# Kernel tuning notes

Hardware: AMD Instinct MI355X
Metric: run time of the kernel (lower is better)

Reference implementation:

```python
import jax, jax.numpy as jnp
import numpy as np

B = 16384
IN_DIM = 28 * 28
HID = 768
NUM_EXPERTS = 8
NUM_CLASSES = 10
H_PHASOR = 32          # phasor bank harmonics -> 2*H features
DELTA0 = 7.0
DECAY = 0.7            # spiking attention leak
THETA = 1.0
K_WINNERS = 5
TOP_K_ROUTE = 2
TRAITS = (0.6, 0.6, 0.5, 0.5, 0.4)


def setup_inputs() -> dict:
    key = jax.random.key(0)
    ks = jax.random.split(key, 16)
    s = 0.02
    return {
        "x": jax.random.normal(ks[0], (B, 28, 28), jnp.float32),
        "W_in": jax.random.normal(ks[1], (IN_DIM, HID), jnp.float32) * s,
        "b_in": jnp.zeros((HID,), jnp.float32),
        "W_ph": jax.random.normal(ks[2], (2 * H_PHASOR, HID), jnp.float32) * s,
        "b_ph": jnp.zeros((HID,), jnp.float32),
        "W_gate": jax.random.normal(ks[3], (HID, NUM_EXPERTS), jnp.float32) * s,
        "b_gate": jnp.zeros((NUM_EXPERTS,), jnp.float32),
        "W_exp": jax.random.normal(ks[4], (NUM_EXPERTS, HID, HID), jnp.float32) * s,
        "b_exp": jnp.zeros((NUM_EXPERTS, HID), jnp.float32),
        "W_th": jax.random.normal(ks[5], (HID, NUM_EXPERTS), jnp.float32) * s,
        "b_th": jnp.zeros((NUM_EXPERTS,), jnp.float32),
        "W_pm": jax.random.normal(ks[6], (5, NUM_EXPERTS), jnp.float32) * s,
        "b_pm": jnp.zeros((NUM_EXPERTS,), jnp.float32),
        "W_out": jax.random.normal(ks[7], (HID, NUM_CLASSES), jnp.float32) * s,
        "b_out": jnp.zeros((NUM_CLASSES,), jnp.float32),
    }


def reference(x, W_in, b_in, W_ph, b_ph, W_gate, b_gate, W_exp, b_exp,
              W_th, b_th, W_pm, b_pm, W_out, b_out):
    Bn = x.shape[0]
    x_flat = x.reshape((Bn, -1))
    proj = x_flat @ W_in + b_in                                  # [B, HID]

    # Phasor bank on per-sample mean activation: sin/cos at H harmonics
    x_mean = jnp.mean(proj, axis=-1)                             # [B]
    freqs = DELTA0 * jnp.arange(1, H_PHASOR + 1, dtype=proj.dtype)
    phase = x_mean[:, None] * freqs[None, :]                     # [B, H]
    feats = jnp.concatenate([jnp.sin(phase), jnp.cos(phase)], -1)  # [B, 2H]
    enhanced = proj + feats @ W_ph + b_ph                        # [B, HID]

    # Top-K index selection feeding gather/scatter spiking attention
    V = enhanced.shape[-1]
    K = min(32, V)
    topk_idx = jax.lax.top_k(enhanced, K)[1].astype(jnp.int32)   # [B, K]
    w = DECAY ** jnp.arange(K, dtype=enhanced.dtype)             # decaying drive

    def gains_fn(idx):
        v = jnp.zeros((V,), enhanced.dtype).at[idx].add(w)       # scatter-add
        vals, widx = jax.lax.top_k(v, K_WINNERS)                 # k-WTA
        return jnp.ones((V,), enhanced.dtype).at[widx].add(vals / THETA)

    gains = jax.vmap(gains_fn)(topk_idx)                         # [B, V]
    attended = enhanced * gains

    # Personality bias + thalamic bias (thalamic_scale = 1.0)
    traits = jnp.asarray(TRAITS, dtype=enhanced.dtype)
    pbias = traits @ W_pm + b_pm                                 # [E]
    thal = jnp.mean(attended, axis=0) @ W_th + b_th              # [E]

    # MoE retrieval core: gate -> top-k softmax route -> combine experts
    gate_logits = attended @ W_gate + b_gate + pbias[None] + thal[None]  # [B, E]
    gvals, gidx = jax.lax.top_k(gate_logits, TOP_K_ROUTE)        # [B, k]
    gw = jax.nn.softmax(gvals, axis=-1)                          # [B, k]
    exp_out = jnp.einsum('bh,ehd->bed', attended, W_exp) + b_exp[None]   # [B, E, HID]
    sel = jnp.take_along_axis(exp_out, gidx[:, :, None], axis=1)  # [B, k, HID]
    context = jnp.sum(gw[:, :, None] * sel, axis=1)              # [B, HID]

    return context @ W_out + b_out                               # [B, classes]
```

## Files before the change

### kernel.cpp

```cpp
#include <hip/hip_runtime.h>
#include <hip/hip_bf16.h>
#include <cstddef>

#define BATCH 16384
#define IND   784
#define HID   768
#define NEXP  8
#define KT13  13

typedef short bf16x8 __attribute__((ext_vector_type(8)));
typedef float f32x4  __attribute__((ext_vector_type(4)));
typedef unsigned short ushort_t;

#define GLD16(g, l)                                                            \
  __builtin_amdgcn_global_load_lds(                                            \
      (const __attribute__((address_space(1))) unsigned int*)(g),              \
      (__attribute__((address_space(3))) unsigned int*)(l), 16, 0, 0)

__global__ __launch_bounds__(256) void k_wtrans(const float* __restrict__ Wexp,
                                                __hip_bfloat16* __restrict__ Wt)
{
  __shared__ float tile[32][33];
  const int e = blockIdx.z;
  const int h0 = blockIdx.x * 32, d0 = blockIdx.y * 32;
  const int tx = threadIdx.x & 31, ty = threadIdx.x >> 5;
  const float* src = Wexp + ((size_t)e * HID + h0) * HID + d0;
  #pragma unroll
  for (int i = 0; i < 4; i++)
    tile[ty + 8 * i][tx] = src[(size_t)(ty + 8 * i) * HID + tx];
  __syncthreads();
  __hip_bfloat16* dst = Wt + ((size_t)e * HID + d0) * HID + h0;
  #pragma unroll
  for (int i = 0; i < 4; i++)
    dst[(size_t)(ty + 8 * i) * HID + tx] = __float2bfloat16(tile[tx][ty + 8 * i]);
}

__device__ inline ushort_t bf16_rne(float f) {
  union { float f; unsigned u; } v; v.f = f;
  unsigned r = v.u + 0x7fffu + ((v.u >> 16) & 1u);
  return (ushort_t)(r >> 16);
}
__device__ inline float bf16_to_f(ushort_t h) {
  union { unsigned u; float f; } v; v.u = ((unsigned)h) << 16;
  return v.f;
}

__global__ __launch_bounds__(256) void k_packA(const float* __restrict__ x,
                                               ushort_t* __restrict__ Ahi,
                                               ushort_t* __restrict__ Alo)
{
  const int kt = blockIdx.x, mt = blockIdx.y;
  const size_t tbase = ((size_t)mt * KT13 + kt) * 8192;
  const int kb = kt * 64;
  #pragma unroll
  for (int i = 0; i < 4; i++) {
    int id = i * 256 + threadIdx.x;
    int r = id >> 3, c = id & 7;
    int row = mt * 128 + r;
    int k0 = kb + c * 8;
    float v[8];
    if (k0 + 8 <= IND) {
      const float4* p = reinterpret_cast<const float4*>(x + (size_t)row * IND + k0);
      float4 a = p[0], b = p[1];
      v[0] = a.x; v[1] = a.y; v[2] = a.z; v[3] = a.w;
      v[4] = b.x; v[5] = b.y; v[6] = b.z; v[7] = b.w;
    } else {
      #pragma unroll
      for (int j = 0; j < 8; j++) v[j] = (k0 + j < IND) ? x[(size_t)row * IND + k0 + j] : 0.f;
    }
    ushort_t hi[8], lo[8];
    #pragma unroll
    for (int j = 0; j < 8; j++) {
      hi[j] = bf16_rne(v[j]);
      lo[j] = bf16_rne(v[j] - bf16_to_f(hi[j]));
    }
    size_t dst = tbase + (size_t)r * 64 + ((c ^ (r & 7)) * 8);
    *reinterpret_cast<uint4*>(Ahi + dst) = *reinterpret_cast<uint4*>(hi);
    *reinterpret_cast<uint4*>(Alo + dst) = *reinterpret_cast<uint4*>(lo);
  }
}

__global__ __launch_bounds__(256) void k_packB(const float* __restrict__ W,
                                               ushort_t* __restrict__ Bhi,
                                               ushort_t* __restrict__ Blo)
{
  const int kt = blockIdx.x, nt = blockIdx.y;
  const size_t tbase = ((size_t)nt * KT13 + kt) * 8192;
  const int kb = kt * 64;
  #pragma unroll
  for (int i = 0; i < 4; i++) {
    int id = i * 256 + threadIdx.x;
    int r = id >> 3, c = id & 7;
    int n = nt * 128 + r;
    int k0 = kb + c * 8;
    float v[8];
    #pragma unroll
    for (int j = 0; j < 8; j++)
      v[j] = (k0 + j < IND) ? W[(size_t)(k0 + j) * HID + n] : 0.f;
    ushort_t hi[8], lo[8];
    #pragma unroll
    for (int j = 0; j < 8; j++) {
      hi[j] = bf16_rne(v[j]);
      lo[j] = bf16_rne(v[j] - bf16_to_f(hi[j]));
    }
    size_t dst = tbase + (size_t)r * 64 + ((c ^ (r & 7)) * 8);
    *reinterpret_cast<uint4*>(Bhi + dst) = *reinterpret_cast<uint4*>(hi);
    *reinterpret_cast<uint4*>(Blo + dst) = *reinterpret_cast<uint4*>(lo);
  }
}

__global__ __launch_bounds__(256, 2) void k_proj2(const ushort_t* __restrict__ Ahi,
                                                  const ushort_t* __restrict__ Alo,
                                                  const ushort_t* __restrict__ Bhi,
                                                  const ushort_t* __restrict__ Blo,
                                                  const float* __restrict__ bias,
                                                  float* __restrict__ out,
                                                  float* __restrict__ pm)
{
  __shared__ __align__(16) ushort_t lds[4 * 8192];
  const int bid = blockIdx.x;
  const int sid = (bid & 7) * 96 + (bid >> 3);
  const int mt = sid / 6, nt = sid - 6 * mt;
  const int tid = threadIdx.x, lane = tid & 63, w = tid >> 6;
  const int m0 = (w >> 1) * 64, n0 = (w & 1) * 64;
  const int l15 = lane & 15, g = lane >> 4;

  f32x4 acc[4][4];
  #pragma unroll
  for (int i = 0; i < 4; i++)
    #pragma unroll
    for (int j = 0; j < 4; j++) acc[i][j] = (f32x4){0.f, 0.f, 0.f, 0.f};

  const size_t abase = (size_t)mt * KT13 * 8192;
  const size_t bbase = (size_t)nt * KT13 * 8192;

  for (int kt = 0; kt < KT13; kt++) {
    __syncthreads();
    const ushort_t* srcs[4] = { Ahi + abase + (size_t)kt * 8192,
                                Alo + abase + (size_t)kt * 8192,
                                Bhi + bbase + (size_t)kt * 8192,
                                Blo + bbase + (size_t)kt * 8192 };
    #pragma unroll
    for (int buf = 0; buf < 4; buf++) {
      #pragma unroll
      for (int i = 0; i < 4; i++) {
        int off = w * 2048 + i * 512 + lane * 8;
        GLD16(srcs[buf] + off, &lds[buf * 8192 + w * 2048 + i * 512]);
      }
    }
    asm volatile("s_waitcnt vmcnt(0)");
    __syncthreads();
    #pragma unroll
    for (int ks = 0; ks < 2; ks++) {
      bf16x8 ah[4], al[4], bh[4], bl[4];
      #pragma unroll
      for (int i = 0; i < 4; i++) {
        int ca = ((4 * ks + g) ^ (l15 & 7)) * 8;
        int ra = m0 + 16 * i + l15;
        ah[i] = *reinterpret_cast<const bf16x8*>(&lds[0 * 8192 + ra * 64 + ca]);
        al[i] = *reinterpret_cast<const bf16x8*>(&lds[1 * 8192 + ra * 64 + ca]);
        int rb = n0 + 16 * i + l15;
        bh[i] = *reinterpret_cast<const bf16x8*>(&lds[2 * 8192 + rb * 64 + ca]);
        bl[i] = *reinterpret_cast<const bf16x8*>(&lds[3 * 8192 + rb * 64 + ca]);
      }
      #pragma unroll
      for (int i = 0; i < 4; i++)
        #pragma unroll
        for (int j = 0; j < 4; j++) {
          acc[i][j] = __builtin_amdgcn_mfma_f32_16x16x32_bf16(ah[i], bh[j], acc[i][j], 0, 0, 0);
          acc[i][j] = __builtin_amdgcn_mfma_f32_16x16x32_bf16(ah[i], bl[j], acc[i][j], 0, 0, 0);
          acc[i][j] = __builtin_amdgcn_mfma_f32_16x16x32_bf16(al[i], bh[j], acc[i][j], 0, 0, 0);
        }
    }
  }
  float bl[4];
  #pragma unroll
  for (int j = 0; j < 4; j++) bl[j] = bias[nt * 128 + n0 + 16 * j + l15];
  #pragma unroll
  for (int i = 0; i < 4; i++) {
    #pragma unroll
    for (int q = 0; q < 4; q++) {
      int m = mt * 128 + m0 + 16 * i + g * 4 + q;
      #pragma unroll
      for (int j = 0; j < 4; j++) {
        int n = nt * 128 + n0 + 16 * j + l15;
        out[(size_t)m * HID + n] = acc[i][j][q] + bl[j];
      }
    }
  }
  const float blsum = bl[0] + bl[1] + bl[2] + bl[3];
  const size_t pslot = (size_t)(nt * 2 + (w & 1)) * BATCH;
  #pragma unroll
  for (int i = 0; i < 4; i++) {
    #pragma unroll
    for (int q = 0; q < 4; q++) {
      float s = acc[i][0][q] + acc[i][1][q] + acc[i][2][q] + acc[i][3][q] + blsum;
      s += __shfl_xor(s, 1); s += __shfl_xor(s, 2);
      s += __shfl_xor(s, 4); s += __shfl_xor(s, 8);
      if (l15 == 0)
        pm[pslot + mt * 128 + m0 + 16 * i + g * 4 + q] = s;
    }
  }
}

__global__ __launch_bounds__(256) void k_phasor(const float* __restrict__ pm,
                                                const float* __restrict__ Wph,
                                                const float* __restrict__ bph,
                                                float* __restrict__ enh)
{
  __shared__ float Fs[64][132];
  __shared__ float Ws[64][128];
  __shared__ float mlds[128];
  const int t  = threadIdx.x;
  const int bm = blockIdx.y * 128, bn = blockIdx.x * 128;
  if (t < 128) {
    float s = 0.f;
    #pragma unroll
    for (int k = 0; k < 12; k++) s += pm[(size_t)k * BATCH + bm + t];
    mlds[t] = s * (1.0f / 768.0f);
  }
  __syncthreads();
  {
    const int r = t >> 1;
    const float mn = mlds[r];
    if ((t & 1) == 0) {
      #pragma unroll
      for (int j = 0; j < 32; j++) Fs[j][r] = sinf(mn * (7.0f * (j + 1)));
    } else {
      #pragma unroll
      for (int j = 0; j < 32; j++) Fs[32 + j][r] = cosf(mn * (7.0f * (j + 1)));
    }
  }
  #pragma unroll
  for (int i = 0; i < 8; i++) {
    int f4 = i * 256 + t;
    int k = f4 >> 5, n4 = (f4 & 31) * 4;
    *reinterpret_cast<float4*>(&Ws[k][n4]) =
        *reinterpret_cast<const float4*>(Wph + (size_t)k * HID + bn + n4);
  }
  __syncthreads();

  const int m0 = (t >> 4) * 8, n0 = (t & 15) * 8;
  float acc[8][8];
  #pragma unroll
  for (int i = 0; i < 8; i++)
    #pragma unroll
    for (int j = 0; j < 8; j++) acc[i][j] = 0.f;
  #pragma unroll 4
  for (int k = 0; k < 64; k++) {
    float a[8], b[8];
    *reinterpret_cast<float4*>(&a[0]) = *reinterpret_cast<const float4*>(&Fs[k][m0]);
    *reinterpret_cast<float4*>(&a[4]) = *reinterpret_cast<const float4*>(&Fs[k][m0 + 4]);
    *reinterpret_cast<float4*>(&b[0]) = *reinterpret_cast<const float4*>(&Ws[k][n0]);
    *reinterpret_cast<float4*>(&b[4]) = *reinterpret_cast<const float4*>(&Ws[k][n0 + 4]);
    #pragma unroll
    for (int i = 0; i < 8; i++)
      #pragma unroll
      for (int j = 0; j < 8; j++) acc[i][j] = fmaf(a[i], b[j], acc[i][j]);
  }
  float bl[8];
  #pragma unroll
  for (int j = 0; j < 8; j++) bl[j] = bph[bn + n0 + j];
  #pragma unroll
  for (int i = 0; i < 8; i++) {
    float* rowp = enh + (size_t)(bm + m0 + i) * HID + bn + n0;
    float4 p0 = *reinterpret_cast<float4*>(rowp);
    float4 p1 = *reinterpret_cast<float4*>(rowp + 4);
    p0.x += acc[i][0] + bl[0]; p0.y += acc[i][1] + bl[1];
    p0.z += acc[i][2] + bl[2]; p0.w += acc[i][3] + bl[3];
    p1.x += acc[i][4] + bl[4]; p1.y += acc[i][5] + bl[5];
    p1.z += acc[i][6] + bl[6]; p1.w += acc[i][7] + bl[7];
    *reinterpret_cast<float4*>(rowp)     = p0;
    *reinterpret_cast<float4*>(rowp + 4) = p1;
  }
}

__global__ __launch_bounds__(256) void k_attend(const float* __restrict__ enh,
                                                const float* __restrict__ Wg,
                                                __hip_bfloat16* __restrict__ attb,
                                                float* __restrict__ glog,
                                                float* __restrict__ partials)
{
  __shared__ float WgT[8][768];
  __shared__ float cs[4][768];
  const int t = threadIdx.x, lane = t & 63, w = t >> 6;
  for (int i = t; i < 768 * 8; i += 256) { int c = i >> 3, e = i & 7; WgT[e][c] = Wg[i]; }
  for (int i = t; i < 4 * 768; i += 256) cs[i / 768][i % 768] = 0.f;
  __syncthreads();

  for (int rr = 0; rr < 8; ++rr) {
    const int row = blockIdx.x * 32 + rr * 4 + w;
    const float* er = enh + (size_t)row * HID;
    float o[12], s[12];
    #pragma unroll
    for (int j = 0; j < 12; j++) { o[j] = er[lane + 64 * j]; s[j] = o[j]; }

    int wc[5];
    #pragma unroll
    for (int k = 0; k < 5; k++) {
      float v = -3.4e38f; int c = 0x7fffffff;
      #pragma unroll
      for (int j = 0; j < 12; j++)
        if (s[j] > v) { v = s[j]; c = lane + 64 * j; }
      #pragma unroll
      for (int off = 32; off; off >>= 1) {
        float ov = __shfl_xor(v, off); int oc = __shfl_xor(c, off);
        if (ov > v || (ov == v && oc < c)) { v = ov; c = oc; }
      }
      wc[k] = c;
      if (lane == (c & 63)) {
        #pragma unroll
        for (int j = 0; j < 12; j++) if (j == (c >> 6)) s[j] = -3.4e38f;
      }
    }

    float a[12];
    #pragma unroll
    for (int j = 0; j < 12; j++) a[j] = o[j];
    float wv = 1.0f;
    #pragma unroll
    for (int k = 0; k < 5; k++) {
      int c = wc[k];
      if (lane == (c & 63)) {
        #pragma unroll
        for (int j = 0; j < 12; j++) if (j == (c >> 6)) a[j] = o[j] * (1.0f + wv);
      }
      wv *= 0.7f;
    }
    #pragma unroll
    for (int j = 0; j < 12; j++)
      attb[(size_t)row * HID + lane + 64 * j] = __float2bfloat16(a[j]);
    #pragma unroll
    for (int j = 0; j < 12; j++) cs[w][lane + 64 * j] += a[j];

    float p[8];
    #pragma unroll
    for (int e = 0; e < 8; e++) p[e] = 0.f;
    #pragma unroll
    for (int j = 0; j < 12; j++) {
      int c = lane + 64 * j;
      #pragma unroll
      for (int e = 0; e < 8; e++) p[e] = fmaf(a[j], WgT[e][c], p[e]);
    }
    #pragma unroll
    for (int e = 0; e < 8; e++) {
      #pragma unroll
      for (int off = 32; off; off >>= 1) p[e] += __shfl_xor(p[e], off);
    }
    if (lane == 0) {
      #pragma unroll
      for (int e = 0; e < 8; e++) glog[(size_t)row * 8 + e] = p[e];
    }
  }
  __syncthreads();
  for (int i = t; i < 768; i += 256)
    partials[(size_t)blockIdx.x * 768 + i] = cs[0][i] + cs[1][i] + cs[2][i] + cs[3][i];
}

__global__ void k_thal(const float* __restrict__ partials,
                       const float* __restrict__ Wth, const float* __restrict__ bth,
                       const float* __restrict__ Wpm, const float* __restrict__ bpm,
                       const float* __restrict__ bgate, float* __restrict__ add8)
{
  __shared__ float cm[768];
  __shared__ float th[8];
  const int t = threadIdx.x;
  float s = 0.f;
  #pragma unroll 8
  for (int b = 0; b < 512; b++) s += partials[(size_t)b * 768 + t];
  cm[t] = s * (1.0f / 16384.0f);
  __syncthreads();
  if (t < 256) {
    int e = t >> 5, l = t & 31;
    float ps = 0.f;
    for (int c = l; c < 768; c += 32) ps = fmaf(cm[c], Wth[(size_t)c * 8 + e], ps);
    #pragma unroll
    for (int off = 16; off; off >>= 1) ps += __shfl_xor(ps, off);
    if (l == 0) th[e] = ps + bth[e];
  }
  __syncthreads();
  if (t < 8) {
    const float TR[5] = {0.6f, 0.6f, 0.5f, 0.5f, 0.4f};
    float pb = bpm[t];
    #pragma unroll
    for (int i = 0; i < 5; i++) pb = fmaf(TR[i], Wpm[i * 8 + t], pb);
    add8[t] = th[t] + pb + bgate[t];
  }
}

__global__ __launch_bounds__(256) void k_route(const float* __restrict__ glog,
                                               const float* __restrict__ add8,
                                               float* __restrict__ rw,
                                               unsigned char* __restrict__ re,
                                               int* __restrict__ counts)
{
  __shared__ float a8[8];
  __shared__ int lc[8];
  const int t = threadIdx.x;
  if (t < 8) { a8[t] = add8[t]; lc[t] = 0; }
  __syncthreads();
  const int row = blockIdx.x * 256 + t;
  const float4* gp = reinterpret_cast<const float4*>(glog + (size_t)row * 8);
  float4 g0 = gp[0], g1 = gp[1];
  float l[8] = { g0.x + a8[0], g0.y + a8[1], g0.z + a8[2], g0.w + a8[3],
                 g1.x + a8[4], g1.y + a8[5], g1.z + a8[6], g1.w + a8[7] };
  float v0 = l[0], v1 = -3.4e38f; int i0 = 0, i1 = 0;
  #pragma unroll
  for (int e = 1; e < 8; e++) {
    if (l[e] > v0)      { v1 = v0; i1 = i0; v0 = l[e]; i0 = e; }
    else if (l[e] > v1) { v1 = l[e]; i1 = e; }
  }
  float ex = expf(v1 - v0);
  float inv = 1.0f / (1.0f + ex);
  rw[row * 2] = inv; rw[row * 2 + 1] = ex * inv;
  re[row * 2] = (unsigned char)i0; re[row * 2 + 1] = (unsigned char)i1;
  atomicAdd(&lc[i0], 1); atomicAdd(&lc[i1], 1);
  __syncthreads();
  if (t < 8) atomicAdd(&counts[t], lc[t]);
}

__global__ void k_prefix(const int* __restrict__ counts, int* __restrict__ meta)
{
  if (threadIdx.x == 0) {
    int o = 0, tt = 0;
    for (int e = 0; e < 8; e++) {
      meta[e] = o; meta[9 + e] = tt; meta[19 + e] = o;
      o += counts[e]; tt += (counts[e] + 127) >> 7;
    }
    meta[8] = o; meta[17] = tt; meta[18] = tt;
  }
}

__global__ __launch_bounds__(256) void k_scatter(const unsigned char* __restrict__ re,
                                                 int* __restrict__ meta,
                                                 int* __restrict__ perm,
                                                 int* __restrict__ inv)
{
  __shared__ int lc[8], base[8];
  const int t = threadIdx.x;
  if (t < 8) lc[t] = 0;
  __syncthreads();
  const int row = blockIdx.x * 256 + t;
  const int e0 = re[row * 2], e1 = re[row * 2 + 1];
  const int p0 = atomicAdd(&lc[e0], 1);
  const int p1 = atomicAdd(&lc[e1], 1);
  __syncthreads();
  if (t < 8) base[t] = atomicAdd(&meta[19 + t], lc[t]);
  __syncthreads();
  const int s0 = base[e0] + p0;
  const int s1 = base[e1] + p1;
  perm[s0] = row * 2;     inv[row * 2]     = s0;
  perm[s1] = row * 2 + 1; inv[row * 2 + 1] = s1;
}

__global__ __launch_bounds__(512) void k_expert(const unsigned short* __restrict__ attb,
                                                const unsigned short* __restrict__ Wt,
                                                const float* __restrict__ bexp,
                                                const float* __restrict__ rw,
                                                const int* __restrict__ perm,
                                                const int* __restrict__ meta,
                                                ushort_t* __restrict__ ctxP)
{
  const int l = blockIdx.x;
  const int xcd = l & 7, idx = l >> 3;
  const int tb = xcd + 8 * (idx / 6);
  const int nb = (idx - 6 * (idx / 6)) * 128;
  if (tb >= meta[18]) return;
  __shared__ __align__(16) ushort_t sst[2][2][8192];
  __shared__ int rid[128];
  __shared__ float gws[128];
  __shared__ float bxs[128];

  const int* tst = meta + 9;
  int e = 0;
  #pragma unroll
  for (int i = 1; i < 8; i++) if (tb >= tst[i]) e = i;
  const int tix  = tb - tst[e];
  const int off  = meta[e];
  const int cnt  = meta[e + 1] - off;
  const int rbase = off + tix * 128;
  const int vcnt  = min(128, cnt - tix * 128);
  const int tid = threadIdx.x;

  if (tid < 128) {
    if (tid < vcnt) {
      int p = perm[rbase + tid];
      rid[tid] = p >> 1; gws[tid] = rw[p];
    } else {
      rid[tid] = 0; gws[tid] = 0.f;
    }
    bxs[tid] = bexp[(size_t)e * HID + nb + tid];
  }
  __syncthreads();

  const int lane = tid & 63, w = tid >> 6;
  const int m0 = (w >> 2) * 64, n0 = (w & 3) * 32;
  const int l15 = lane & 15, g = lane >> 4;
  const unsigned short* wbase = Wt + ((size_t)e * HID + nb) * HID;

  const int chr = tid >> 3;
  const int sc  = ((tid & 7) ^ (chr & 7)) * 8;
  const int ra0 = rid[chr], ra1 = rid[chr + 64];
  const ushort_t* asrc0 = attb  + (size_t)ra0 * HID + sc;
  const ushort_t* asrc1 = attb  + (size_t)ra1 * HID + sc;
  const ushort_t* bsrc0 = wbase + (size_t)chr * HID + sc;
  const ushort_t* bsrc1 = wbase + (size_t)(chr + 64) * HID + sc;
  const int dst0 = (0 * 512 + w * 64) * 8;
  const int dst1 = (1 * 512 + w * 64) * 8;

#define ESTAGE(kb, b)                                                          \
  { GLD16(asrc0 + (kb), &sst[b][0][dst0]);                                     \
    GLD16(asrc1 + (kb), &sst[b][0][dst1]);                                     \
    GLD16(bsrc0 + (kb), &sst[b][1][dst0]);                                     \
    GLD16(bsrc1 + (kb), &sst[b][1][dst1]); }

  f32x4 acc[4][2];
  #pragma unroll
  for (int i = 0; i < 4; i++)
    #pragma unroll
    for (int j = 0; j < 2; j++) acc[i][j] = (f32x4){0.f, 0.f, 0.f, 0.f};

  ESTAGE(0, 0);
  for (int t = 0; t < 12; t++) {
    const int cb = t & 1;
    if (t < 11) {
      ESTAGE((t + 1) * 64, cb ^ 1);
      asm volatile("s_waitcnt vmcnt(4)" ::: "memory");
    } else {
      asm volatile("s_waitcnt vmcnt(0)" ::: "memory");
    }
    __builtin_amdgcn_s_barrier();
    const ushort_t* As = &sst[cb][0][0];
    const ushort_t* Bs = &sst[cb][1][0];
    #pragma unroll
    for (int ks = 0; ks < 2; ks++) {
      bf16x8 af[4], bfr[2];
      #pragma unroll
      for (int i = 0; i < 4; i++) {
        int ca = (((4 * ks + g) ^ (l15 & 7)) * 8);
        af[i] = *reinterpret_cast<const bf16x8*>(As + (m0 + 16 * i + l15) * 64 + ca);
      }
      #pragma unroll
      for (int j = 0; j < 2; j++) {
        int ca = (((4 * ks + g) ^ (l15 & 7)) * 8);
        bfr[j] = *reinterpret_cast<const bf16x8*>(Bs + (n0 + 16 * j + l15) * 64 + ca);
      }
      #pragma unroll
      for (int i = 0; i < 4; i++)
        #pragma unroll
        for (int j = 0; j < 2; j++)
          acc[i][j] = __builtin_amdgcn_mfma_f32_16x16x32_bf16(af[i], bfr[j], acc[i][j], 0, 0, 0);
    }
    __builtin_amdgcn_s_barrier();
  }
#undef ESTAGE

  unsigned short* Cs = &sst[0][0][0];
  __syncthreads();
  #pragma unroll
  for (int i = 0; i < 4; i++) {
    #pragma unroll
    for (int q = 0; q < 4; q++) {
      int m = m0 + 16 * i + g * 4 + q;
      float gwv = gws[m];
      #pragma unroll
      for (int j = 0; j < 2; j++) {
        int n = n0 + 16 * j + l15;
        Cs[m * 128 + n] = bf16_rne(gwv * (acc[i][j][q] + bxs[n]));
      }
    }
  }
  __syncthreads();
  #pragma unroll
  for (int c = 0; c < 4; c++) {
    int r = w * 16 + c * 4 + (lane >> 4);
    if (r < vcnt) {
      uint4 v = *reinterpret_cast<const uint4*>(Cs + r * 128 + l15 * 8);
      *reinterpret_cast<uint4*>(ctxP + (size_t)(rbase + r) * HID + nb + l15 * 8) = v;
    }
  }
}

__global__ __launch_bounds__(256) void k_out(const ushort_t* __restrict__ ctxP,
                                             const int* __restrict__ inv,
                                             const float* __restrict__ Wout,
                                             const float* __restrict__ bout,
                                             float* __restrict__ out)
{
  __shared__ float wT[10][768];
  const int t = threadIdx.x, lane = t & 63, w = t >> 6;
  for (int i = t; i < 7680; i += 256) { int cl = i / 768, d = i - cl * 768; wT[cl][d] = Wout[(size_t)d * 10 + cl]; }
  __syncthreads();
  for (int rr = 0; rr < 8; ++rr) {
    const int row = blockIdx.x * 32 + rr * 4 + w;
    const int s0 = inv[row * 2], s1 = inv[row * 2 + 1];
    const ushort_t* p0 = ctxP + (size_t)s0 * HID;
    const ushort_t* p1 = ctxP + (size_t)s1 * HID;
    float cd[12];
    #pragma unroll
    for (int j = 0; j < 12; j++)
      cd[j] = bf16_to_f(p0[lane + 64 * j]) + bf16_to_f(p1[lane + 64 * j]);
    float p[10];
    #pragma unroll
    for (int cl = 0; cl < 10; cl++) {
      float ps = 0.f;
      #pragma unroll
      for (int j = 0; j < 12; j++) ps = fmaf(cd[j], wT[cl][lane + 64 * j], ps);
      #pragma unroll
      for (int off = 32; off; off >>= 1) ps += __shfl_xor(ps, off);
      p[cl] = ps;
    }
    if (lane == 0) {
      #pragma unroll
      for (int cl = 0; cl < 10; cl++) out[(size_t)row * 10 + cl] = p[cl] + bout[cl];
    }
  }
}

extern "C" void kernel_launch(void* const* d_in, const int* in_sizes, int n_in,
                              void* d_out, int out_size, void* d_ws, size_t ws_size,
                              hipStream_t stream)
{
  const float* x     = (const float*)d_in[0];
  const float* W_in  = (const float*)d_in[1];
  const float* b_in  = (const float*)d_in[2];
  const float* W_ph  = (const float*)d_in[3];
  const float* b_ph  = (const float*)d_in[4];
  const float* W_g   = (const float*)d_in[5];
  const float* b_g   = (const float*)d_in[6];
  const float* W_exp = (const float*)d_in[7];
  const float* b_exp = (const float*)d_in[8];
  const float* W_th  = (const float*)d_in[9];
  const float* b_th  = (const float*)d_in[10];
  const float* W_pm  = (const float*)d_in[11];
  const float* b_pm  = (const float*)d_in[12];
  const float* W_out = (const float*)d_in[13];
  const float* b_out = (const float*)d_in[14];
  float* out = (float*)d_out;

  char* ws = (char*)d_ws;
  size_t off = 0;
  float* enh = (float*)(ws + off); off += (size_t)BATCH * HID * 4;
  char*  r1  = ws + off;           off += (size_t)2 * BATCH * KT13 * 64 * 2;
  ushort_t* Ahi = (ushort_t*)r1;
  ushort_t* Alo = Ahi + (size_t)BATCH * KT13 * 64;
  __hip_bfloat16* attb = (__hip_bfloat16*)r1;
  __hip_bfloat16* Wt   = (__hip_bfloat16*)(r1 + (size_t)BATCH * HID * 2);
  float* glog     = (float*)(ws + off); off += (size_t)BATCH * 8 * 4;
  float* partials = (float*)(ws + off); off += (size_t)512 * 768 * 4;
  float* pm       = (float*)(ws + off); off += (size_t)12 * BATCH * 4;
  float* add8     = (float*)(ws + off); off += 256;
  float* rw       = (float*)(ws + off); off += (size_t)BATCH * 2 * 4;
  unsigned char* re = (unsigned char*)(ws + off); off += (size_t)BATCH * 2;
  int* counts = (int*)(ws + off); off += 256;
  int* meta   = (int*)(ws + off); off += 256;
  int* perm   = (int*)(ws + off); off += (size_t)BATCH * 2 * 4;
  int* invp   = (int*)(ws + off); off += (size_t)BATCH * 2 * 4;
  ushort_t* Bhi = (ushort_t*)(ws + off); off += (size_t)KT13 * 64 * HID * 2;
  ushort_t* Blo = (ushort_t*)(ws + off); off += (size_t)KT13 * 64 * HID * 2;
  ushort_t* ctxP = (ushort_t*)enh;

  hipMemsetAsync(counts, 0, 32, stream);
  k_packB <<<dim3(13, 6),     256, 0, stream>>>(W_in, Bhi, Blo);
  k_packA <<<dim3(13, 128),   256, 0, stream>>>(x, Ahi, Alo);
  k_proj2 <<<768,             256, 0, stream>>>(Ahi, Alo, Bhi, Blo, b_in, enh, pm);
  k_wtrans<<<dim3(24, 24, 8), 256, 0, stream>>>(W_exp, Wt);
  k_phasor<<<dim3(6, 128),    256, 0, stream>>>(pm, W_ph, b_ph, enh);
  k_attend<<<512,             256, 0, stream>>>(enh, W_g, attb, glog, partials);
  k_thal  <<<1,               768, 0, stream>>>(partials, W_th, b_th, W_pm, b_pm, b_g, add8);
  k_route <<<64,              256, 0, stream>>>(glog, add8, rw, re, counts);
  k_prefix<<<1,                64, 0, stream>>>(counts, meta);
  k_scatter<<<64,             256, 0, stream>>>(re, meta, perm, invp);
  k_expert<<<1584,            512, 0, stream>>>((const unsigned short*)attb, (const unsigned short*)Wt,
                                                b_exp, rw, perm, meta, ctxP);
  k_out   <<<512,             256, 0, stream>>>(ctxP, invp, W_out, b_out, out);
}
```

Measured before the change: 309.0 us.

## Double-buffer the projection GEMM with 512 threads and simplify expert-kernel sync

The split-bf16 projection GEMM now uses 8 waves per block with LDS double buffering, so the next K tile is fetched while the current one is multiplied. Each wave owns a 64x32 sub-tile, which halves its accumulator registers and doubles the per-row partial-sum slots that the phasor kernel reduces. The expert kernel swaps its manual vmcnt waits plus raw barriers for plain __syncthreads after each tile. This trades hand-tuned wait counts for compiler-managed syncs, and the doubled LDS footprint (128KB) may cap resident blocks per CU.

```diff
diff --git a/kernel.cpp b/kernel.cpp
--- a/kernel.cpp
+++ b/kernel.cpp
@@ -109,92 +109,101 @@
   }
 }
 
-__global__ __launch_bounds__(256, 2) void k_proj2(const ushort_t* __restrict__ Ahi,
-                                                  const ushort_t* __restrict__ Alo,
-                                                  const ushort_t* __restrict__ Bhi,
-                                                  const ushort_t* __restrict__ Blo,
-                                                  const float* __restrict__ bias,
-                                                  float* __restrict__ out,
-                                                  float* __restrict__ pm)
-{
-  __shared__ __align__(16) ushort_t lds[4 * 8192];
+__global__ __launch_bounds__(512) void k_proj2(const ushort_t* __restrict__ Ahi,
+                                               const ushort_t* __restrict__ Alo,
+                                               const ushort_t* __restrict__ Bhi,
+                                               const ushort_t* __restrict__ Blo,
+                                               const float* __restrict__ bias,
+                                               float* __restrict__ out,
+                                               float* __restrict__ pm)
+{
+  __shared__ __align__(16) ushort_t lds[2][4][8192];
   const int bid = blockIdx.x;
   const int sid = (bid & 7) * 96 + (bid >> 3);
   const int mt = sid / 6, nt = sid - 6 * mt;
   const int tid = threadIdx.x, lane = tid & 63, w = tid >> 6;
-  const int m0 = (w >> 1) * 64, n0 = (w & 1) * 64;
+  const int m0 = (w >> 2) * 64, n0 = (w & 3) * 32;
   const int l15 = lane & 15, g = lane >> 4;
 
-  f32x4 acc[4][4];
+  const ushort_t* tAh = Ahi + (size_t)mt * KT13 * 8192;
+  const ushort_t* tAl = Alo + (size_t)mt * KT13 * 8192;
+  const ushort_t* tBh = Bhi + (size_t)nt * KT13 * 8192;
+  const ushort_t* tBl = Blo + (size_t)nt * KT13 * 8192;
+  const int soff = w * 1024 + lane * 8;
+  const int doff = w * 1024;
+
+#define PSTAGE(kt, b)                                                          \
+  { _Pragma("unroll")                                                          \
+    for (int i = 0; i < 2; i++) {                                              \
+      GLD16(tAh + (size_t)(kt) * 8192 + soff + i * 512, &lds[b][0][doff + i * 512]); \
+      GLD16(tAl + (size_t)(kt) * 8192 + soff + i * 512, &lds[b][1][doff + i * 512]); \
+      GLD16(tBh + (size_t)(kt) * 8192 + soff + i * 512, &lds[b][2][doff + i * 512]); \
+      GLD16(tBl + (size_t)(kt) * 8192 + soff + i * 512, &lds[b][3][doff + i * 512]); \
+    } }
+
+  f32x4 acc[4][2];
   #pragma unroll
   for (int i = 0; i < 4; i++)
     #pragma unroll
-    for (int j = 0; j < 4; j++) acc[i][j] = (f32x4){0.f, 0.f, 0.f, 0.f};
-
-  const size_t abase = (size_t)mt * KT13 * 8192;
-  const size_t bbase = (size_t)nt * KT13 * 8192;
-
+    for (int j = 0; j < 2; j++) acc[i][j] = (f32x4){0.f, 0.f, 0.f, 0.f};
+
+  PSTAGE(0, 0);
+  __syncthreads();
   for (int kt = 0; kt < KT13; kt++) {
-    __syncthreads();
-    const ushort_t* srcs[4] = { Ahi + abase + (size_t)kt * 8192,
-                                Alo + abase + (size_t)kt * 8192,
-                                Bhi + bbase + (size_t)kt * 8192,
-                                Blo + bbase + (size_t)kt * 8192 };
-    #pragma unroll
-    for (int buf = 0; buf < 4; buf++) {
-      #pragma unroll
-      for (int i = 0; i < 4; i++) {
-        int off = w * 2048 + i * 512 + lane * 8;
-        GLD16(srcs[buf] + off, &lds[buf * 8192 + w * 2048 + i * 512]);
-      }
-    }
-    asm volatile("s_waitcnt vmcnt(0)");
-    __syncthreads();
+    const int cb = kt & 1;
+    if (kt < KT13 - 1) PSTAGE(kt + 1, cb ^ 1);
     #pragma unroll
     for (int ks = 0; ks < 2; ks++) {
-      bf16x8 ah[4], al[4], bh[4], bl[4];
+      bf16x8 ah[4], al[4], bh[2], blv[2];
       #pragma unroll
       for (int i = 0; i < 4; i++) {
         int ca = ((4 * ks + g) ^ (l15 & 7)) * 8;
         int ra = m0 + 16 * i + l15;
-        ah[i] = *reinterpret_cast<const bf16x8*>(&lds[0 * 8192 + ra * 64 + ca]);
-        al[i] = *reinterpret_cast<const bf16x8*>(&lds[1 * 8192 + ra * 64 + ca]);
-        int rb = n0 + 16 * i + l15;
-        bh[i] = *reinterpret_cast<const bf16x8*>(&lds[2 * 8192 + rb * 64 + ca]);
-        bl[i] = *reinterpret_cast<const bf16x8*>(&lds[3 * 8192 + rb * 64 + ca]);
+        ah[i] = *reinterpret_cast<const bf16x8*>(&lds[cb][0][ra * 64 + ca]);
+        al[i] = *reinterpret_cast<const bf16x8*>(&lds[cb][1][ra * 64 + ca]);
+      }
+      #pragma unroll
+      for (int j = 0; j < 2; j++) {
+        int ca = ((4 * ks + g) ^ (l15 & 7)) * 8;
+        int rb = n0 + 16 * j + l15;
+        bh[j]  = *reinterpret_cast<const bf16x8*>(&lds[cb][2][rb * 64 + ca]);
+        blv[j] = *reinterpret_cast<const bf16x8*>(&lds[cb][3][rb * 64 + ca]);
       }
       #pragma unroll
       for (int i = 0; i < 4; i++)
         #pragma unroll
-        for (int j = 0; j < 4; j++) {
-          acc[i][j] = __builtin_amdgcn_mfma_f32_16x16x32_bf16(ah[i], bh[j], acc[i][j], 0, 0, 0);
-          acc[i][j] = __builtin_amdgcn_mfma_f32_16x16x32_bf16(ah[i], bl[j], acc[i][j], 0, 0, 0);
-          acc[i][j] = __builtin_amdgcn_mfma_f32_16x16x32_bf16(al[i], bh[j], acc[i][j], 0, 0, 0);
+        for (int j = 0; j < 2; j++) {
+          acc[i][j] = __builtin_amdgcn_mfma_f32_16x16x32_bf16(ah[i], bh[j],  acc[i][j], 0, 0, 0);
+          acc[i][j] = __builtin_amdgcn_mfma_f32_16x16x32_bf16(ah[i], blv[j], acc[i][j], 0, 0, 0);
+          acc[i][j] = __builtin_amdgcn_mfma_f32_16x16x32_bf16(al[i], bh[j],  acc[i][j], 0, 0, 0);
         }
     }
-  }
-  float bl[4];
-  #pragma unroll
-  for (int j = 0; j < 4; j++) bl[j] = bias[nt * 128 + n0 + 16 * j + l15];
+    __syncthreads();
+  }
+#undef PSTAGE
+
+  float bv[2];
+  #pragma unroll
+  for (int j = 0; j < 2; j++) bv[j] = bias[nt * 128 + n0 + 16 * j + l15];
   #pragma unroll
   for (int i = 0; i < 4; i++) {
     #pragma unroll
     for (int q = 0; q < 4; q++) {
       int m = mt * 128 + m0 + 16 * i + g * 4 + q;
       #pragma unroll
-      for (int j = 0; j < 4; j++) {
+      for (int j = 0; j < 2; j++) {
         int n = nt * 128 + n0 + 16 * j + l15;
-        out[(size_t)m * HID + n] = acc[i][j][q] + bl[j];
-      }
-    }
-  }
-  const float blsum = bl[0] + bl[1] + bl[2] + bl[3];
-  const size_t pslot = (size_t)(nt * 2 + (w & 1)) * BATCH;
+        out[(size_t)m * HID + n] = acc[i][j][q] + bv[j];
+      }
+    }
+  }
+  const float bvsum = bv[0] + bv[1];
+  const size_t pslot = (size_t)(nt * 4 + (w & 3)) * BATCH;
   #pragma unroll
   for (int i = 0; i < 4; i++) {
     #pragma unroll
     for (int q = 0; q < 4; q++) {
-      float s = acc[i][0][q] + acc[i][1][q] + acc[i][2][q] + acc[i][3][q] + blsum;
+      float s = acc[i][0][q] + acc[i][1][q] + bvsum;
       s += __shfl_xor(s, 1); s += __shfl_xor(s, 2);
       s += __shfl_xor(s, 4); s += __shfl_xor(s, 8);
       if (l15 == 0)
@@ -216,7 +225,7 @@
   if (t < 128) {
     float s = 0.f;
     #pragma unroll
-    for (int k = 0; k < 12; k++) s += pm[(size_t)k * BATCH + bm + t];
+    for (int k = 0; k < 24; k++) s += pm[(size_t)k * BATCH + bm + t];
     mlds[t] = s * (1.0f / 768.0f);
   }
   __syncthreads();
@@ -521,15 +530,10 @@
     for (int j = 0; j < 2; j++) acc[i][j] = (f32x4){0.f, 0.f, 0.f, 0.f};
 
   ESTAGE(0, 0);
+  __syncthreads();
   for (int t = 0; t < 12; t++) {
     const int cb = t & 1;
-    if (t < 11) {
-      ESTAGE((t + 1) * 64, cb ^ 1);
-      asm volatile("s_waitcnt vmcnt(4)" ::: "memory");
-    } else {
-      asm volatile("s_waitcnt vmcnt(0)" ::: "memory");
-    }
-    __builtin_amdgcn_s_barrier();
+    if (t < 11) ESTAGE((t + 1) * 64, cb ^ 1);
     const ushort_t* As = &sst[cb][0][0];
     const ushort_t* Bs = &sst[cb][1][0];
     #pragma unroll
@@ -551,12 +555,11 @@
         for (int j = 0; j < 2; j++)
           acc[i][j] = __builtin_amdgcn_mfma_f32_16x16x32_bf16(af[i], bfr[j], acc[i][j], 0, 0, 0);
     }
-    __builtin_amdgcn_s_barrier();
+    __syncthreads();
   }
 #undef ESTAGE
 
   unsigned short* Cs = &sst[0][0][0];
-  __syncthreads();
   #pragma unroll
   for (int i = 0; i < 4; i++) {
     #pragma unroll
@@ -648,7 +651,7 @@
   __hip_bfloat16* Wt   = (__hip_bfloat16*)(r1 + (size_t)BATCH * HID * 2);
   float* glog     = (float*)(ws + off); off += (size_t)BATCH * 8 * 4;
   float* partials = (float*)(ws + off); off += (size_t)512 * 768 * 4;
-  float* pm       = (float*)(ws + off); off += (size_t)12 * BATCH * 4;
+  float* pm       = (float*)(ws + off); off += (size_t)24 * BATCH * 4;
   float* add8     = (float*)(ws + off); off += 256;
   float* rw       = (float*)(ws + off); off += (size_t)BATCH * 2 * 4;
   unsigned char* re = (unsigned char*)(ws + off); off += (size_t)BATCH * 2;
@@ -663,7 +666,7 @@
   hipMemsetAsync(counts, 0, 32, stream);
   k_packB <<<dim3(13, 6),     256, 0, stream>>>(W_in, Bhi, Blo);
   k_packA <<<dim3(13, 128),   256, 0, stream>>>(x, Ahi, Alo);
-  k_proj2 <<<768,             256, 0, stream>>>(Ahi, Alo, Bhi, Blo, b_in, enh, pm);
+  k_proj2 <<<768,             512, 0, stream>>>(Ahi, Alo, Bhi, Blo, b_in, enh, pm);
   k_wtrans<<<dim3(24, 24, 8), 256, 0, stream>>>(W_exp, Wt);
   k_phasor<<<dim3(6, 128),    256, 0, stream>>>(pm, W_ph, b_ph, enh);
   k_attend<<<512,             256, 0, stream>>>(enh, W_g, attb, glog, partials);
```

Measured after the change: 317.3 us. 2.7% more time.

## Replace double-buffered K=64 expert GEMM loop with single-buffered K=128 stages

Applied to the files above, without the earlier changes.

The expert GEMM kernel drops its two-stage LDS double buffer with K=64 slices and instead loads a single K=128 slice per iteration (six iterations), waiting for all loads before computing. Shared memory stays the same size and a launch-bounds hint of two blocks per CU is added, so occupancy from other resident blocks is meant to hide load latency instead of in-block prefetch. It halves the number of barrier rounds but gives up overlap of loads with MFMA work inside each block.

```diff
diff --git a/kernel.cpp b/kernel.cpp
--- a/kernel.cpp
+++ b/kernel.cpp
@@ -453,20 +453,20 @@
   perm[s1] = row * 2 + 1; inv[row * 2 + 1] = s1;
 }
 
-__global__ __launch_bounds__(512) void k_expert(const unsigned short* __restrict__ attb,
-                                                const unsigned short* __restrict__ Wt,
-                                                const float* __restrict__ bexp,
-                                                const float* __restrict__ rw,
-                                                const int* __restrict__ perm,
-                                                const int* __restrict__ meta,
-                                                ushort_t* __restrict__ ctxP)
+__global__ __launch_bounds__(512, 2) void k_expert(const ushort_t* __restrict__ attb,
+                                                   const ushort_t* __restrict__ Wt,
+                                                   const float* __restrict__ bexp,
+                                                   const float* __restrict__ rw,
+                                                   const int* __restrict__ perm,
+                                                   const int* __restrict__ meta,
+                                                   ushort_t* __restrict__ ctxP)
 {
   const int l = blockIdx.x;
   const int xcd = l & 7, idx = l >> 3;
   const int tb = xcd + 8 * (idx / 6);
   const int nb = (idx - 6 * (idx / 6)) * 128;
   if (tb >= meta[18]) return;
-  __shared__ __align__(16) ushort_t sst[2][2][8192];
+  __shared__ __align__(16) ushort_t sst[2][16384];
   __shared__ int rid[128];
   __shared__ float gws[128];
   __shared__ float bxs[128];
@@ -496,23 +496,33 @@
   const int lane = tid & 63, w = tid >> 6;
   const int m0 = (w >> 2) * 64, n0 = (w & 3) * 32;
   const int l15 = lane & 15, g = lane >> 4;
-  const unsigned short* wbase = Wt + ((size_t)e * HID + nb) * HID;
-
-  const int chr = tid >> 3;
-  const int sc  = ((tid & 7) ^ (chr & 7)) * 8;
-  const int ra0 = rid[chr], ra1 = rid[chr + 64];
-  const ushort_t* asrc0 = attb  + (size_t)ra0 * HID + sc;
-  const ushort_t* asrc1 = attb  + (size_t)ra1 * HID + sc;
-  const ushort_t* bsrc0 = wbase + (size_t)chr * HID + sc;
-  const ushort_t* bsrc1 = wbase + (size_t)(chr + 64) * HID + sc;
-  const int dst0 = (0 * 512 + w * 64) * 8;
-  const int dst1 = (1 * 512 + w * 64) * 8;
-
-#define ESTAGE(kb, b)                                                          \
-  { GLD16(asrc0 + (kb), &sst[b][0][dst0]);                                     \
-    GLD16(asrc1 + (kb), &sst[b][0][dst1]);                                     \
-    GLD16(bsrc0 + (kb), &sst[b][1][dst0]);                                     \
-    GLD16(bsrc1 + (kb), &sst[b][1][dst1]); }
+  const ushort_t* wbase = Wt + ((size_t)e * HID + nb) * HID;
+
+  const int srow = tid >> 4;
+  const int c0  = tid & 15;
+  const int sc  = (c0 >> 3) * 64 + (((c0 & 7) ^ (srow & 7)) * 8);
+  const ushort_t* asrc0 = attb + (size_t)rid[srow      ] * HID + sc;
+  const ushort_t* asrc1 = attb + (size_t)rid[srow + 32 ] * HID + sc;
+  const ushort_t* asrc2 = attb + (size_t)rid[srow + 64 ] * HID + sc;
+  const ushort_t* asrc3 = attb + (size_t)rid[srow + 96 ] * HID + sc;
+  const ushort_t* bsrc0 = wbase + (size_t)(srow      ) * HID + sc;
+  const ushort_t* bsrc1 = wbase + (size_t)(srow + 32 ) * HID + sc;
+  const ushort_t* bsrc2 = wbase + (size_t)(srow + 64 ) * HID + sc;
+  const ushort_t* bsrc3 = wbase + (size_t)(srow + 96 ) * HID + sc;
+  const int d0 = (0 * 512 + w * 64) * 8;
+  const int d1 = (1 * 512 + w * 64) * 8;
+  const int d2 = (2 * 512 + w * 64) * 8;
+  const int d3 = (3 * 512 + w * 64) * 8;
+
+#define ESTAGE(kb)                                                             \
+  { GLD16(asrc0 + (kb), &sst[0][d0]);                                          \
+    GLD16(asrc1 + (kb), &sst[0][d1]);                                          \
+    GLD16(asrc2 + (kb), &sst[0][d2]);                                          \
+    GLD16(asrc3 + (kb), &sst[0][d3]);                                          \
+    GLD16(bsrc0 + (kb), &sst[1][d0]);                                          \
+    GLD16(bsrc1 + (kb), &sst[1][d1]);                                          \
+    GLD16(bsrc2 + (kb), &sst[1][d2]);                                          \
+    GLD16(bsrc3 + (kb), &sst[1][d3]); }
 
   f32x4 acc[4][2];
   #pragma unroll
@@ -520,30 +530,25 @@
     #pragma unroll
     for (int j = 0; j < 2; j++) acc[i][j] = (f32x4){0.f, 0.f, 0.f, 0.f};
 
-  ESTAGE(0, 0);
-  for (int t = 0; t < 12; t++) {
-    const int cb = t & 1;
-    if (t < 11) {
-      ESTAGE((t + 1) * 64, cb ^ 1);
-      asm volatile("s_waitcnt vmcnt(4)" ::: "memory");
-    } else {
-      asm volatile("s_waitcnt vmcnt(0)" ::: "memory");
-    }
-    __builtin_amdgcn_s_barrier();
-    const ushort_t* As = &sst[cb][0][0];
-    const ushort_t* Bs = &sst[cb][1][0];
-    #pragma unroll
-    for (int ks = 0; ks < 2; ks++) {
+  for (int t = 0; t < 6; t++) {
+    __syncthreads();
+    ESTAGE(t * 128);
+    asm volatile("s_waitcnt vmcnt(0)");
+    __syncthreads();
+    #pragma unroll
+    for (int ks = 0; ks < 4; ks++) {
+      const int kh2 = (ks >> 1) * 64;
+      const int kk  = 4 * (ks & 1) + g;
       bf16x8 af[4], bfr[2];
       #pragma unroll
       for (int i = 0; i < 4; i++) {
-        int ca = (((4 * ks + g) ^ (l15 & 7)) * 8);
-        af[i] = *reinterpret_cast<const bf16x8*>(As + (m0 + 16 * i + l15) * 64 + ca);
+        int ra = m0 + 16 * i + l15;
+        af[i] = *reinterpret_cast<const bf16x8*>(&sst[0][ra * 128 + kh2 + ((kk ^ (ra & 7)) * 8)]);
       }
       #pragma unroll
       for (int j = 0; j < 2; j++) {
-        int ca = (((4 * ks + g) ^ (l15 & 7)) * 8);
-        bfr[j] = *reinterpret_cast<const bf16x8*>(Bs + (n0 + 16 * j + l15) * 64 + ca);
+        int rb = n0 + 16 * j + l15;
+        bfr[j] = *reinterpret_cast<const bf16x8*>(&sst[1][rb * 128 + kh2 + ((kk ^ (rb & 7)) * 8)]);
       }
       #pragma unroll
       for (int i = 0; i < 4; i++)
@@ -551,12 +556,11 @@
         for (int j = 0; j < 2; j++)
           acc[i][j] = __builtin_amdgcn_mfma_f32_16x16x32_bf16(af[i], bfr[j], acc[i][j], 0, 0, 0);
     }
-    __builtin_amdgcn_s_barrier();
   }
 #undef ESTAGE
 
-  unsigned short* Cs = &sst[0][0][0];
-  __syncthreads();
+  __syncthreads();
+  ushort_t* Cs = &sst[0][0];
   #pragma unroll
   for (int i = 0; i < 4; i++) {
     #pragma unroll
@@ -671,7 +675,7 @@
   k_route <<<64,              256, 0, stream>>>(glog, add8, rw, re, counts);
   k_prefix<<<1,                64, 0, stream>>>(counts, meta);
   k_scatter<<<64,             256, 0, stream>>>(re, meta, perm, invp);
-  k_expert<<<1584,            512, 0, stream>>>((const unsigned short*)attb, (const unsigned short*)Wt,
+  k_expert<<<1584,            512, 0, stream>>>((const ushort_t*)attb, (const ushort_t*)Wt,
                                                 b_exp, rw, perm, meta, ctxP);
   k_out   <<<512,             256, 0, stream>>>(ctxP, invp, W_out, b_out, out);
 }
```

Measured after the change: 319.8 us. 1.04x slower.

## Fuse output projection into expert GEMM epilogue, emit per-slice class partials

Applied to the files above, without the earlier changes.

The expert kernel no longer writes the full bf16 context tile to global memory. Its epilogue multiplies the tile by the matching 128-row slice of W_out in LDS and writes 10-class partial sums per routed row and column slice. A small k_out2 kernel then adds the 6 slices and the 2 routes per sample, plus the bias. This removes the large context write and re-read. The main loop also drops the hand-tuned vmcnt waits and split barriers in favour of plain __syncthreads, which may reduce overlap between loads and MFMA.

```diff
diff --git a/kernel.cpp b/kernel.cpp
--- a/kernel.cpp
+++ b/kernel.cpp
@@ -453,20 +453,22 @@
   perm[s1] = row * 2 + 1; inv[row * 2 + 1] = s1;
 }
 
-__global__ __launch_bounds__(512) void k_expert(const unsigned short* __restrict__ attb,
-                                                const unsigned short* __restrict__ Wt,
+__global__ __launch_bounds__(512) void k_expert(const ushort_t* __restrict__ attb,
+                                                const ushort_t* __restrict__ Wt,
                                                 const float* __restrict__ bexp,
                                                 const float* __restrict__ rw,
                                                 const int* __restrict__ perm,
                                                 const int* __restrict__ meta,
-                                                ushort_t* __restrict__ ctxP)
+                                                const float* __restrict__ Wout,
+                                                float* __restrict__ pog)
 {
   const int l = blockIdx.x;
   const int xcd = l & 7, idx = l >> 3;
   const int tb = xcd + 8 * (idx / 6);
-  const int nb = (idx - 6 * (idx / 6)) * 128;
+  const int nbq = idx - 6 * (idx / 6);
+  const int nb = nbq * 128;
   if (tb >= meta[18]) return;
-  __shared__ __align__(16) ushort_t sst[2][2][8192];
+  __shared__ __align__(16) ushort_t sst[32768];
   __shared__ int rid[128];
   __shared__ float gws[128];
   __shared__ float bxs[128];
@@ -496,23 +498,22 @@
   const int lane = tid & 63, w = tid >> 6;
   const int m0 = (w >> 2) * 64, n0 = (w & 3) * 32;
   const int l15 = lane & 15, g = lane >> 4;
-  const unsigned short* wbase = Wt + ((size_t)e * HID + nb) * HID;
+  const ushort_t* wbase = Wt + ((size_t)e * HID + nb) * HID;
 
   const int chr = tid >> 3;
   const int sc  = ((tid & 7) ^ (chr & 7)) * 8;
-  const int ra0 = rid[chr], ra1 = rid[chr + 64];
-  const ushort_t* asrc0 = attb  + (size_t)ra0 * HID + sc;
-  const ushort_t* asrc1 = attb  + (size_t)ra1 * HID + sc;
+  const ushort_t* asrc0 = attb  + (size_t)rid[chr] * HID + sc;
+  const ushort_t* asrc1 = attb  + (size_t)rid[chr + 64] * HID + sc;
   const ushort_t* bsrc0 = wbase + (size_t)chr * HID + sc;
   const ushort_t* bsrc1 = wbase + (size_t)(chr + 64) * HID + sc;
   const int dst0 = (0 * 512 + w * 64) * 8;
   const int dst1 = (1 * 512 + w * 64) * 8;
 
 #define ESTAGE(kb, b)                                                          \
-  { GLD16(asrc0 + (kb), &sst[b][0][dst0]);                                     \
-    GLD16(asrc1 + (kb), &sst[b][0][dst1]);                                     \
-    GLD16(bsrc0 + (kb), &sst[b][1][dst0]);                                     \
-    GLD16(bsrc1 + (kb), &sst[b][1][dst1]); }
+  { GLD16(asrc0 + (kb), &sst[(b) * 16384 + dst0]);                             \
+    GLD16(asrc1 + (kb), &sst[(b) * 16384 + dst1]);                             \
+    GLD16(bsrc0 + (kb), &sst[(b) * 16384 + 8192 + dst0]);                      \
+    GLD16(bsrc1 + (kb), &sst[(b) * 16384 + 8192 + dst1]); }
 
   f32x4 acc[4][2];
   #pragma unroll
@@ -521,17 +522,12 @@
     for (int j = 0; j < 2; j++) acc[i][j] = (f32x4){0.f, 0.f, 0.f, 0.f};
 
   ESTAGE(0, 0);
+  __syncthreads();
   for (int t = 0; t < 12; t++) {
     const int cb = t & 1;
-    if (t < 11) {
-      ESTAGE((t + 1) * 64, cb ^ 1);
-      asm volatile("s_waitcnt vmcnt(4)" ::: "memory");
-    } else {
-      asm volatile("s_waitcnt vmcnt(0)" ::: "memory");
-    }
-    __builtin_amdgcn_s_barrier();
-    const ushort_t* As = &sst[cb][0][0];
-    const ushort_t* Bs = &sst[cb][1][0];
+    if (t < 11) ESTAGE((t + 1) * 64, cb ^ 1);
+    const ushort_t* As = &sst[cb * 16384];
+    const ushort_t* Bs = &sst[cb * 16384 + 8192];
     #pragma unroll
     for (int ks = 0; ks < 2; ks++) {
       bf16x8 af[4], bfr[2];
@@ -551,12 +547,14 @@
         for (int j = 0; j < 2; j++)
           acc[i][j] = __builtin_amdgcn_mfma_f32_16x16x32_bf16(af[i], bfr[j], acc[i][j], 0, 0, 0);
     }
-    __builtin_amdgcn_s_barrier();
+    __syncthreads();
   }
 #undef ESTAGE
 
-  unsigned short* Cs = &sst[0][0][0];
-  __syncthreads();
+  ushort_t* Cs  = sst;
+  float* wlds   = reinterpret_cast<float*>(sst + 17408);
+  float* po     = wlds + 1280;
+  for (int i = tid; i < 1280; i += 512) wlds[i] = Wout[nb * 10 + i];
   #pragma unroll
   for (int i = 0; i < 4; i++) {
     #pragma unroll
@@ -566,55 +564,57 @@
       #pragma unroll
       for (int j = 0; j < 2; j++) {
         int n = n0 + 16 * j + l15;
-        Cs[m * 128 + n] = bf16_rne(gwv * (acc[i][j][q] + bxs[n]));
-      }
-    }
-  }
-  __syncthreads();
-  #pragma unroll
-  for (int c = 0; c < 4; c++) {
-    int r = w * 16 + c * 4 + (lane >> 4);
+        Cs[m * 132 + n] = bf16_rne(gwv * (acc[i][j][q] + bxs[n]));
+      }
+    }
+  }
+  __syncthreads();
+  {
+    const int r = tid >> 2, nq = tid & 3;
+    float s[10];
+    #pragma unroll
+    for (int cl = 0; cl < 10; cl++) s[cl] = 0.f;
+    #pragma unroll
+    for (int kk = 0; kk < 32; kk++) {
+      int k = (kk + r) & 31;
+      float cv = bf16_to_f(Cs[r * 132 + nq * 32 + k]);
+      const float* wp = &wlds[(nq * 32 + k) * 10];
+      #pragma unroll
+      for (int cl = 0; cl < 10; cl++) s[cl] = fmaf(cv, wp[cl], s[cl]);
+    }
+    #pragma unroll
+    for (int cl = 0; cl < 10; cl++) po[(r * 4 + nq) * 10 + cl] = s[cl];
+  }
+  __syncthreads();
+  for (int i = tid; i < 1280; i += 512) {
+    int r = i / 10, cl = i - r * 10;
     if (r < vcnt) {
-      uint4 v = *reinterpret_cast<const uint4*>(Cs + r * 128 + l15 * 8);
-      *reinterpret_cast<uint4*>(ctxP + (size_t)(rbase + r) * HID + nb + l15 * 8) = v;
-    }
-  }
-}
-
-__global__ __launch_bounds__(256) void k_out(const ushort_t* __restrict__ ctxP,
-                                             const int* __restrict__ inv,
-                                             const float* __restrict__ Wout,
-                                             const float* __restrict__ bout,
-                                             float* __restrict__ out)
-{
-  __shared__ float wT[10][768];
-  const int t = threadIdx.x, lane = t & 63, w = t >> 6;
-  for (int i = t; i < 7680; i += 256) { int cl = i / 768, d = i - cl * 768; wT[cl][d] = Wout[(size_t)d * 10 + cl]; }
-  __syncthreads();
-  for (int rr = 0; rr < 8; ++rr) {
-    const int row = blockIdx.x * 32 + rr * 4 + w;
-    const int s0 = inv[row * 2], s1 = inv[row * 2 + 1];
-    const ushort_t* p0 = ctxP + (size_t)s0 * HID;
-    const ushort_t* p1 = ctxP + (size_t)s1 * HID;
-    float cd[12];
-    #pragma unroll
-    for (int j = 0; j < 12; j++)
-      cd[j] = bf16_to_f(p0[lane + 64 * j]) + bf16_to_f(p1[lane + 64 * j]);
-    float p[10];
-    #pragma unroll
-    for (int cl = 0; cl < 10; cl++) {
-      float ps = 0.f;
-      #pragma unroll
-      for (int j = 0; j < 12; j++) ps = fmaf(cd[j], wT[cl][lane + 64 * j], ps);
-      #pragma unroll
-      for (int off = 32; off; off >>= 1) ps += __shfl_xor(ps, off);
-      p[cl] = ps;
-    }
-    if (lane == 0) {
-      #pragma unroll
-      for (int cl = 0; cl < 10; cl++) out[(size_t)row * 10 + cl] = p[cl] + bout[cl];
-    }
-  }
+      float v = (po[(r * 4 + 0) * 10 + cl] + po[(r * 4 + 1) * 10 + cl]) +
+                (po[(r * 4 + 2) * 10 + cl] + po[(r * 4 + 3) * 10 + cl]);
+      pog[((size_t)nbq * 32768 + rbase + r) * 10 + cl] = v;
+    }
+  }
+}
+
+__global__ __launch_bounds__(256) void k_out2(const float* __restrict__ pog,
+                                              const int* __restrict__ inv,
+                                              const float* __restrict__ bout,
+                                              float* __restrict__ out)
+{
+  const int row = blockIdx.x * 256 + threadIdx.x;
+  const int s0 = inv[row * 2], s1 = inv[row * 2 + 1];
+  float acc[10];
+  #pragma unroll
+  for (int cl = 0; cl < 10; cl++) acc[cl] = bout[cl];
+  #pragma unroll
+  for (int q = 0; q < 6; q++) {
+    const float* p0 = &pog[((size_t)q * 32768 + s0) * 10];
+    const float* p1 = &pog[((size_t)q * 32768 + s1) * 10];
+    #pragma unroll
+    for (int cl = 0; cl < 10; cl++) acc[cl] += p0[cl] + p1[cl];
+  }
+  #pragma unroll
+  for (int cl = 0; cl < 10; cl++) out[(size_t)row * 10 + cl] = acc[cl];
 }
 
 extern "C" void kernel_launch(void* const* d_in, const int* in_sizes, int n_in,
@@ -658,7 +658,7 @@
   int* invp   = (int*)(ws + off); off += (size_t)BATCH * 2 * 4;
   ushort_t* Bhi = (ushort_t*)(ws + off); off += (size_t)KT13 * 64 * HID * 2;
   ushort_t* Blo = (ushort_t*)(ws + off); off += (size_t)KT13 * 64 * HID * 2;
-  ushort_t* ctxP = (ushort_t*)enh;
+  float* pog = enh;
 
   hipMemsetAsync(counts, 0, 32, stream);
   k_packB <<<dim3(13, 6),     256, 0, stream>>>(W_in, Bhi, Blo);
@@ -671,7 +671,7 @@
   k_route <<<64,              256, 0, stream>>>(glog, add8, rw, re, counts);
   k_prefix<<<1,                64, 0, stream>>>(counts, meta);
   k_scatter<<<64,             256, 0, stream>>>(re, meta, perm, invp);
-  k_expert<<<1584,            512, 0, stream>>>((const unsigned short*)attb, (const unsigned short*)Wt,
-                                                b_exp, rw, perm, meta, ctxP);
-  k_out   <<<512,             256, 0, stream>>>(ctxP, invp, W_out, b_out, out);
-}
+  k_expert<<<1584,            512, 0, stream>>>((const ushort_t*)attb, (const ushort_t*)Wt,
+                                                b_exp, rw, perm, meta, W_out, pog);
+  k_out2  <<<64,              256, 0, stream>>>(pog, invp, b_out, out);
+}
```

New measurement: 343.3 us. 11.1% more time.
